# Kernel tuning notes

Hardware: AMD Instinct MI355X
Metric: run time of the kernel (lower is better)

The kernel has to match this reference:

```python
import jax, jax.numpy as jnp
import numpy as np

IN_FEATURES = 512
OUT_FEATURES = 512
GRID_SIZE = 5
SPLINE_ORDER = 3


def setup_inputs() -> dict:
    key = jax.random.key(0)
    k1, k2 = jax.random.split(key)
    x = jax.random.normal(k1, (8192, IN_FEATURES), dtype=jnp.float32)
    coefficients = jax.random.normal(
        k2, (IN_FEATURES, OUT_FEATURES, GRID_SIZE + SPLINE_ORDER), dtype=jnp.float32) * 0.1
    h = 2.0 / GRID_SIZE
    grid = jnp.linspace(-1.0 - SPLINE_ORDER * h, 1.0 + SPLINE_ORDER * h,
                        GRID_SIZE + 2 * SPLINE_ORDER + 1, dtype=jnp.float32)
    return {"x": x, "coefficients": coefficients, "grid": grid}


def _b_splines(xn, grid, order):
    # xn: (batch, in); grid: (G + 2*order + 1,)
    xe = xn[:, :, None]  # (b, i, 1)
    # k = 0: indicator of knot intervals -> (b, i, G + 2*order)
    B = ((xe >= grid[:-1]) & (xe < grid[1:])).astype(xn.dtype)
    for k in range(1, order + 1):
        left_den = grid[k:-1] - grid[:-k - 1]
        left_den = jnp.where(left_den == 0, jnp.ones_like(left_den), left_den)
        left = (xe - grid[:-k - 1]) / left_den * B[:, :, :-1]
        right_den = grid[k + 1:] - grid[1:-k]
        right_den = jnp.where(right_den == 0, jnp.ones_like(right_den), right_den)
        right = (grid[k + 1:] - xe) / right_den * B[:, :, 1:]
        B = left + right
    return B  # (b, i, G + order)


def reference(x, coefficients, grid):
    xn = jnp.tanh(x)
    bases = _b_splines(xn, grid, SPLINE_ORDER)  # (b, i, k)
    # replaces the double python loop: sum_i sum_k bases[b,i,k] * coeff[i,o,k]
    return jnp.einsum('bik,iok->bo', bases, coefficients)
```

## Files before the change

kernel.cpp:

```cpp
#include <hip/hip_runtime.h>
#include <hip/hip_bf16.h>
#include <stdint.h>


typedef short s16x8 __attribute__((ext_vector_type(8)));
typedef float f32x4 __attribute__((ext_vector_type(4)));

#define BATCH 8192
#define IN_F  512
#define OUT_F 512
#define NB    8
#define KKTOT (IN_F * NB)
#define BM 64
#define BN 128
#define BK 64
#define NITER (IN_F / NB)

__device__ __forceinline__ uint32_t f2bf(float f) {
    union { float f; uint32_t u; } v; v.f = f;
    return (v.u + 0x7FFFu + ((v.u >> 16) & 1u)) >> 16;
}

__device__ __forceinline__ uint32_t bf16bits(float a) {
    __hip_bfloat16 h = __float2bfloat16(a);
    union { __hip_bfloat16 h; unsigned short u; } c; c.h = h;
    return (uint32_t)c.u;
}

__device__ __forceinline__ s16x8 u4_to_s8(uint4 v) {
    union { uint4 u; s16x8 s; } c; c.u = v; return c.s;
}

__device__ __forceinline__ uint4 bspline_pack(float xraw) {
    float e  = __expf(2.0f * xraw);
    float xn = 1.0f - 2.0f / (e + 1.0f);
    float u  = __fmaf_rn(xn, 2.5f, 5.5f);
    float fj = floorf(u);
    fj = fminf(fmaxf(fj, 3.0f), 7.0f);
    float t  = u - fj;
    float omt = 1.0f - t;
    float t2 = t * t;
    float t3 = t2 * t;
    const float s = 0.16666666666666666f;
    float w0 = s * omt * omt * omt;
    float w3 = s * t3;
    float w1 = s * __fmaf_rn(3.0f, t3, __fmaf_rn(-6.0f, t2, 4.0f));
    float w2 = 1.0f - w0 - w1 - w3;
    uint64_t packed = (uint64_t)(bf16bits(w0) | (bf16bits(w1) << 16))
                    | ((uint64_t)(bf16bits(w2) | (bf16bits(w3) << 16)) << 32);
    int sh = ((int)fj - 3) * 16;
    uint64_t lo, hi;
    if (sh == 0)      { lo = packed;       hi = 0ull; }
    else if (sh < 64) { lo = packed << sh; hi = packed >> (64 - sh); }
    else              { lo = 0ull;         hi = packed; }
    return make_uint4((uint32_t)lo, (uint32_t)(lo >> 32),
                      (uint32_t)hi, (uint32_t)(hi >> 32));
}

__global__ __launch_bounds__(256)
void prep_bt(const float* __restrict__ C, unsigned short* __restrict__ BtT) {
    int t = blockIdx.x * 256 + threadIdx.x;
    int o = t & (OUT_F - 1);
    int i = t >> 9;
    const float4* src = (const float4*)(C + ((size_t)i * OUT_F + o) * NB);
    float4 c0 = src[0];
    float4 c1 = src[1];
    uint4 val;
    val.x = f2bf(c0.x) | (f2bf(c0.y) << 16);
    val.y = f2bf(c0.z) | (f2bf(c0.w) << 16);
    val.z = f2bf(c1.x) | (f2bf(c1.y) << 16);
    val.w = f2bf(c1.z) | (f2bf(c1.w) << 16);
    *(uint4*)(BtT + (size_t)o * KKTOT + (size_t)i * NB) = val;
}

__device__ __forceinline__ void gload_lds16(const void* g, void* l) {
    __builtin_amdgcn_global_load_lds(
        (const __attribute__((address_space(1))) uint32_t*)g,
        (__attribute__((address_space(3))) uint32_t*)l, 16, 0, 0);
}

__global__ __launch_bounds__(256, 2)
void kan_gemm(const float* __restrict__ X, const unsigned short* __restrict__ BtT,
              float* __restrict__ Out) {
    __shared__ unsigned short Bs[4][8192];

    const int tid    = threadIdx.x;
    const int lane   = tid & 63;
    const int wv     = tid >> 6;
    const int lane16 = lane & 15;
    const int quad   = lane >> 4;

    const int row0 = blockIdx.y * BM;
    const int col0 = blockIdx.x * BN;

    const float* xrow = X + (size_t)(row0 + wv * 16 + lane16) * IN_F;

    const int jg = (lane & 7) ^ ((lane >> 3) & 7);
    const char* gstage = (const char*)BtT
        + ((size_t)(col0 + wv * 8 + (lane >> 3))) * (KKTOT * 2)
        + (size_t)jg * 16;

    const int cbyte = lane16 * 128;
    const int sx0 = ((quad)     ^ (lane16 & 7)) << 4;
    const int sx1 = ((4 + quad) ^ (lane16 & 7)) << 4;

    f32x4 acc[8] = {};
    float xs0a, xs0b, xs1a, xs1b, xs2a, xs2b, xs3a, xs3b;

#define STAGE(BUF, T)                                                         \
    do {                                                                      \
        _Pragma("unroll")                                                     \
        for (int r = 0; r < 4; ++r)                                           \
            gload_lds16(gstage + (size_t)r * 32 * (KKTOT * 2) + (size_t)(T) * 128, \
                        (char*)&Bs[BUF][0] + r * 4096 + wv * 1024);           \
    } while (0)

    STAGE(0, 0);
    xs0a = xrow[quad];  xs0b = xrow[4 + quad];
    STAGE(1, 1);
    xs1a = xrow[8 + quad];  xs1b = xrow[12 + quad];
    asm volatile("s_waitcnt vmcnt(6)" ::: "memory");
    __builtin_amdgcn_s_barrier();

#define BODY(T, CUR, PRE, XCA, XCB, XPA, XPB)                                 \
    do {                                                                      \
        if ((T) + 2 < NITER) {                                                \
            STAGE(PRE, (T) + 2);                                              \
            XPA = xrow[((T) + 2) * 8 + quad];                                 \
            XPB = xrow[((T) + 2) * 8 + 4 + quad];                             \
        }                                                                     \
        const char* bsC = (const char*)&Bs[CUR][0];                           \
        {                                                                     \
            s16x8 af0 = u4_to_s8(bspline_pack(XCA));                          \
            _Pragma("unroll")                                                 \
            for (int cn = 0; cn < 8; ++cn) {                                  \
                s16x8 b = *(const s16x8*)(bsC + cn * 2048 + cbyte + sx0);     \
                acc[cn] = __builtin_amdgcn_mfma_f32_16x16x32_bf16(            \
                    af0, b, acc[cn], 0, 0, 0);                                \
            }                                                                 \
        }                                                                     \
        {                                                                     \
            s16x8 af1 = u4_to_s8(bspline_pack(XCB));                          \
            _Pragma("unroll")                                                 \
            for (int cn = 0; cn < 8; ++cn) {                                  \
                s16x8 b = *(const s16x8*)(bsC + cn * 2048 + cbyte + sx1);     \
                acc[cn] = __builtin_amdgcn_mfma_f32_16x16x32_bf16(            \
                    af1, b, acc[cn], 0, 0, 0);                                \
            }                                                                 \
        }                                                                     \
        if ((T) + 2 < NITER)                                                  \
            asm volatile("s_waitcnt vmcnt(6)" ::: "memory");                  \
        else if ((T) + 1 < NITER)                                             \
            asm volatile("s_waitcnt vmcnt(0)" ::: "memory");                  \
        if ((T) + 1 < NITER) __builtin_amdgcn_s_barrier();                    \
    } while (0)

    for (int t = 0; t < NITER; t += 4) {
        BODY(t + 0, 0, 2, xs0a, xs0b, xs2a, xs2b);
        BODY(t + 1, 1, 3, xs1a, xs1b, xs3a, xs3b);
        BODY(t + 2, 2, 0, xs2a, xs2b, xs0a, xs0b);
        BODY(t + 3, 3, 1, xs3a, xs3b, xs1a, xs1b);
    }
#undef BODY
#undef STAGE

    const int orow = row0 + wv * 16 + quad * 4;
    #pragma unroll
    for (int cn = 0; cn < 8; ++cn) {
        float* dst = Out + (size_t)orow * OUT_F + col0 + cn * 16 + lane16;
        #pragma unroll
        for (int r = 0; r < 4; ++r)
            dst[(size_t)r * OUT_F] = acc[cn][r];
    }
}

extern "C" void kernel_launch(void* const* d_in, const int* in_sizes, int n_in,
                              void* d_out, int out_size, void* d_ws, size_t ws_size,
                              hipStream_t stream) {
    const float* X  = (const float*)d_in[0];
    const float* C  = (const float*)d_in[1];
    float* Out = (float*)d_out;
    unsigned short* BtT = (unsigned short*)d_ws;

    prep_bt<<<dim3((IN_F * OUT_F) / 256), 256, 0, stream>>>(C, BtT);
    kan_gemm<<<dim3(OUT_F / BN, BATCH / BM), 256, 0, stream>>>(X, BtT, Out);
}
```

Before: 140.8 us.

## Use 2x2 wave tiling with paired-buffer prefetch in KAN spline GEMM

Reassigns the four waves from a 4x1 row split (16 rows by 128 columns each) to a 2x2 split (32 rows by 64 columns each). Each B fragment read from LDS now feeds two MFMAs, which halves LDS read traffic per MFMA. The cost is that every row's B-spline basis is now computed by two waves instead of one, doubling the tanh and basis arithmetic. The pipeline also changes: two stages are prefetched and consumed per barrier instead of one, so there are half as many barriers but each wait covers a larger batch of loads.

Measured after the change: 162.9 us. 15.7% more time.

```diff
diff --git a/kernel.cpp b/kernel.cpp
--- a/kernel.cpp
+++ b/kernel.cpp
@@ -87,25 +87,28 @@
     const int tid    = threadIdx.x;
     const int lane   = tid & 63;
     const int wv     = tid >> 6;
+    const int wr     = wv >> 1;
+    const int wc     = wv & 1;
     const int lane16 = lane & 15;
     const int quad   = lane >> 4;
 
     const int row0 = blockIdx.y * BM;
     const int col0 = blockIdx.x * BN;
 
-    const float* xrow = X + (size_t)(row0 + wv * 16 + lane16) * IN_F;
+    const float* xrA = X + (size_t)(row0 + wr * 32 + lane16) * IN_F;
+    const float* xrB = xrA + (size_t)16 * IN_F;
 
     const int jg = (lane & 7) ^ ((lane >> 3) & 7);
     const char* gstage = (const char*)BtT
         + ((size_t)(col0 + wv * 8 + (lane >> 3))) * (KKTOT * 2)
         + (size_t)jg * 16;
 
-    const int cbyte = lane16 * 128;
+    const int cwbyte = (wc * 64 + lane16) * 128;
     const int sx0 = ((quad)     ^ (lane16 & 7)) << 4;
     const int sx1 = ((4 + quad) ^ (lane16 & 7)) << 4;
 
-    f32x4 acc[8] = {};
-    float xs0a, xs0b, xs1a, xs1b, xs2a, xs2b, xs3a, xs3b;
+    f32x4 acc[2][4] = {};
+    float4 xv0, xv1, xv2, xv3;
 
 #define STAGE(BUF, T)                                                         \
     do {                                                                      \
@@ -115,62 +118,85 @@
                         (char*)&Bs[BUF][0] + r * 4096 + wv * 1024);           \
     } while (0)
 
-    STAGE(0, 0);
-    xs0a = xrow[quad];  xs0b = xrow[4 + quad];
-    STAGE(1, 1);
-    xs1a = xrow[8 + quad];  xs1b = xrow[12 + quad];
-    asm volatile("s_waitcnt vmcnt(6)" ::: "memory");
+#define XLOAD(XV, T)                                                          \
+    do {                                                                      \
+        XV.x = xrA[(T) * 8 + quad];                                           \
+        XV.y = xrA[(T) * 8 + 4 + quad];                                       \
+        XV.z = xrB[(T) * 8 + quad];                                           \
+        XV.w = xrB[(T) * 8 + 4 + quad];                                       \
+    } while (0)
+
+#define TILE(CUR, XV)                                                         \
+    do {                                                                      \
+        const char* bs_ = (const char*)&Bs[CUR][0] + cwbyte;                  \
+        s16x8 b[4];                                                           \
+        s16x8 af;                                                             \
+        _Pragma("unroll")                                                     \
+        for (int cn = 0; cn < 4; ++cn)                                        \
+            b[cn] = *(const s16x8*)(bs_ + cn * 2048 + sx0);                   \
+        af = u4_to_s8(bspline_pack(XV.x));                                    \
+        _Pragma("unroll")                                                     \
+        for (int cn = 0; cn < 4; ++cn)                                        \
+            acc[0][cn] = __builtin_amdgcn_mfma_f32_16x16x32_bf16(             \
+                af, b[cn], acc[0][cn], 0, 0, 0);                              \
+        af = u4_to_s8(bspline_pack(XV.z));                                    \
+        _Pragma("unroll")                                                     \
+        for (int cn = 0; cn < 4; ++cn)                                        \
+            acc[1][cn] = __builtin_amdgcn_mfma_f32_16x16x32_bf16(             \
+                af, b[cn], acc[1][cn], 0, 0, 0);                              \
+        _Pragma("unroll")                                                     \
+        for (int cn = 0; cn < 4; ++cn)                                        \
+            b[cn] = *(const s16x8*)(bs_ + cn * 2048 + sx1);                   \
+        af = u4_to_s8(bspline_pack(XV.y));                                    \
+        _Pragma("unroll")                                                     \
+        for (int cn = 0; cn < 4; ++cn)                                        \
+            acc[0][cn] = __builtin_amdgcn_mfma_f32_16x16x32_bf16(             \
+                af, b[cn], acc[0][cn], 0, 0, 0);                              \
+        af = u4_to_s8(bspline_pack(XV.w));                                    \
+        _Pragma("unroll")                                                     \
+        for (int cn = 0; cn < 4; ++cn)                                        \
+            acc[1][cn] = __builtin_amdgcn_mfma_f32_16x16x32_bf16(             \
+                af, b[cn], acc[1][cn], 0, 0, 0);                              \
+    } while (0)
+
+    STAGE(0, 0); XLOAD(xv0, 0);
+    STAGE(1, 1); XLOAD(xv1, 1);
+    asm volatile("s_waitcnt vmcnt(4)" ::: "memory");
     __builtin_amdgcn_s_barrier();
 
-#define BODY(T, CUR, PRE, XCA, XCB, XPA, XPB)                                 \
-    do {                                                                      \
-        if ((T) + 2 < NITER) {                                                \
-            STAGE(PRE, (T) + 2);                                              \
-            XPA = xrow[((T) + 2) * 8 + quad];                                 \
-            XPB = xrow[((T) + 2) * 8 + 4 + quad];                             \
-        }                                                                     \
-        const char* bsC = (const char*)&Bs[CUR][0];                           \
-        {                                                                     \
-            s16x8 af0 = u4_to_s8(bspline_pack(XCA));                          \
-            _Pragma("unroll")                                                 \
-            for (int cn = 0; cn < 8; ++cn) {                                  \
-                s16x8 b = *(const s16x8*)(bsC + cn * 2048 + cbyte + sx0);     \
-                acc[cn] = __builtin_amdgcn_mfma_f32_16x16x32_bf16(            \
-                    af0, b, acc[cn], 0, 0, 0);                                \
-            }                                                                 \
-        }                                                                     \
-        {                                                                     \
-            s16x8 af1 = u4_to_s8(bspline_pack(XCB));                          \
-            _Pragma("unroll")                                                 \
-            for (int cn = 0; cn < 8; ++cn) {                                  \
-                s16x8 b = *(const s16x8*)(bsC + cn * 2048 + cbyte + sx1);     \
-                acc[cn] = __builtin_amdgcn_mfma_f32_16x16x32_bf16(            \
-                    af1, b, acc[cn], 0, 0, 0);                                \
-            }                                                                 \
-        }                                                                     \
-        if ((T) + 2 < NITER)                                                  \
-            asm volatile("s_waitcnt vmcnt(6)" ::: "memory");                  \
-        else if ((T) + 1 < NITER)                                             \
-            asm volatile("s_waitcnt vmcnt(0)" ::: "memory");                  \
-        if ((T) + 1 < NITER) __builtin_amdgcn_s_barrier();                    \
-    } while (0)
-
     for (int t = 0; t < NITER; t += 4) {
-        BODY(t + 0, 0, 2, xs0a, xs0b, xs2a, xs2b);
-        BODY(t + 1, 1, 3, xs1a, xs1b, xs3a, xs3b);
-        BODY(t + 2, 2, 0, xs2a, xs2b, xs0a, xs0b);
-        BODY(t + 3, 3, 1, xs3a, xs3b, xs1a, xs1b);
+        STAGE(2, t + 2); XLOAD(xv2, t + 2);
+        STAGE(3, t + 3); XLOAD(xv3, t + 3);
+        TILE(0, xv0);
+        TILE(1, xv1);
+        asm volatile("s_waitcnt vmcnt(4)" ::: "memory");
+        __builtin_amdgcn_s_barrier();
+
+        if (t + 4 < NITER) {
+            STAGE(0, t + 4); XLOAD(xv0, t + 4);
+            STAGE(1, t + 5); XLOAD(xv1, t + 5);
+        }
+        TILE(2, xv2);
+        TILE(3, xv3);
+        if (t + 4 < NITER) {
+            asm volatile("s_waitcnt vmcnt(4)" ::: "memory");
+            __builtin_amdgcn_s_barrier();
+        }
     }
-#undef BODY
+#undef TILE
+#undef XLOAD
 #undef STAGE
 
-    const int orow = row0 + wv * 16 + quad * 4;
     #pragma unroll
-    for (int cn = 0; cn < 8; ++cn) {
-        float* dst = Out + (size_t)orow * OUT_F + col0 + cn * 16 + lane16;
+    for (int rm = 0; rm < 2; ++rm) {
+        const int orow = row0 + wr * 32 + rm * 16 + quad * 4;
         #pragma unroll
-        for (int r = 0; r < 4; ++r)
-            dst[(size_t)r * OUT_F] = acc[cn][r];
+        for (int cn = 0; cn < 4; ++cn) {
+            float* dst = Out + (size_t)orow * OUT_F + col0 + wc * 64 + cn * 16 + lane16;
+            #pragma unroll
+            for (int r = 0; r < 4; ++r)
+                dst[(size_t)r * OUT_F] = acc[rm][cn][r];
+        }
     }
 }
 
```

## Materialize B-spline basis matrix once and run plain bf16 GEMM

Applied to the files above, without the earlier changes.

Adds a pack_a kernel that evaluates the tanh and cubic B-spline basis for every input once and writes a bf16 A matrix (8192x4096) to workspace. A new GEMM kernel then streams both A and B tiles into LDS with a 2x2 wave layout and double buffering. This removes the basis recomputation that the fused kernel did in every block along the output-column dimension. In exchange it adds 64 MB of writes plus reads of the A matrix, and the new GEMM waits on vmcnt(0) each step. The fused kernel is kept as a fallback when the workspace is too small.

Measured after the change: 140.5 us. About the same (-0.2%).

```diff
diff --git a/kernel.cpp b/kernel.cpp
--- a/kernel.cpp
+++ b/kernel.cpp
@@ -73,6 +73,19 @@
     *(uint4*)(BtT + (size_t)o * KKTOT + (size_t)i * NB) = val;
 }
 
+__global__ __launch_bounds__(256)
+void pack_a(const float* __restrict__ X, unsigned short* __restrict__ Abf) {
+    int t = blockIdx.x * 256 + threadIdx.x;
+    int b  = t >> 8;
+    int ip = t & 255;
+    float2 xv = *(const float2*)(X + (size_t)b * IN_F + ip * 2);
+    uint4 p0 = bspline_pack(xv.x);
+    uint4 p1 = bspline_pack(xv.y);
+    unsigned short* dst = Abf + (size_t)b * KKTOT + ip * 16;
+    *(uint4*)(dst)     = p0;
+    *(uint4*)(dst + 8) = p1;
+}
+
 __device__ __forceinline__ void gload_lds16(const void* g, void* l) {
     __builtin_amdgcn_global_load_lds(
         (const __attribute__((address_space(1))) uint32_t*)g,
@@ -80,8 +93,118 @@
 }
 
 __global__ __launch_bounds__(256, 2)
-void kan_gemm(const float* __restrict__ X, const unsigned short* __restrict__ BtT,
-              float* __restrict__ Out) {
+void kan_gemm_mat(const unsigned short* __restrict__ Abf,
+                  const unsigned short* __restrict__ BtT,
+                  float* __restrict__ Out) {
+    __shared__ unsigned short As[2][4096];
+    __shared__ unsigned short Bs[2][8192];
+
+    const int tid    = threadIdx.x;
+    const int lane   = tid & 63;
+    const int wv     = tid >> 6;
+    const int wr     = wv >> 1;
+    const int wc     = wv & 1;
+    const int lane16 = lane & 15;
+    const int quad   = lane >> 4;
+
+    const int row0 = blockIdx.y * BM;
+    const int col0 = blockIdx.x * BN;
+
+    const int jg = (lane & 7) ^ ((lane >> 3) & 7);
+    const char* gstageB = (const char*)BtT
+        + ((size_t)(col0 + wv * 8 + (lane >> 3))) * (KKTOT * 2)
+        + (size_t)jg * 16;
+    const char* gstageA = (const char*)Abf
+        + ((size_t)(row0 + wv * 8 + (lane >> 3))) * (KKTOT * 2)
+        + (size_t)jg * 16;
+
+    const int cwbyte = (wc * 64 + lane16) * 128;
+    const int arbyte = (wr * 32 + lane16) * 128;
+    const int sx0 = ((quad)     ^ (lane16 & 7)) << 4;
+    const int sx1 = ((4 + quad) ^ (lane16 & 7)) << 4;
+
+    f32x4 acc[2][4] = {};
+
+#define STAGE(BUF, T)                                                         \
+    do {                                                                      \
+        _Pragma("unroll")                                                     \
+        for (int r = 0; r < 4; ++r)                                           \
+            gload_lds16(gstageB + (size_t)r * 32 * (KKTOT * 2) + (size_t)(T) * 128, \
+                        (char*)&Bs[BUF][0] + r * 4096 + wv * 1024);           \
+        gload_lds16(gstageA + (size_t)(T) * 128,                              \
+                    (char*)&As[BUF][0] + wv * 1024);                          \
+        gload_lds16(gstageA + (size_t)32 * (KKTOT * 2) + (size_t)(T) * 128,   \
+                    (char*)&As[BUF][0] + 4096 + wv * 1024);                   \
+    } while (0)
+
+#define TILE(CUR)                                                             \
+    do {                                                                      \
+        const char* bs_ = (const char*)&Bs[CUR][0] + cwbyte;                  \
+        const char* as_ = (const char*)&As[CUR][0] + arbyte;                  \
+        s16x8 b0, b1, b2, b3, af0, af1;                                       \
+        af0 = *(const s16x8*)(as_ + sx0);                                     \
+        af1 = *(const s16x8*)(as_ + 2048 + sx0);                              \
+        b0 = *(const s16x8*)(bs_ + 0 * 2048 + sx0);                           \
+        b1 = *(const s16x8*)(bs_ + 1 * 2048 + sx0);                           \
+        b2 = *(const s16x8*)(bs_ + 2 * 2048 + sx0);                           \
+        b3 = *(const s16x8*)(bs_ + 3 * 2048 + sx0);                           \
+        acc[0][0] = __builtin_amdgcn_mfma_f32_16x16x32_bf16(af0, b0, acc[0][0], 0, 0, 0); \
+        acc[0][1] = __builtin_amdgcn_mfma_f32_16x16x32_bf16(af0, b1, acc[0][1], 0, 0, 0); \
+        acc[0][2] = __builtin_amdgcn_mfma_f32_16x16x32_bf16(af0, b2, acc[0][2], 0, 0, 0); \
+        acc[0][3] = __builtin_amdgcn_mfma_f32_16x16x32_bf16(af0, b3, acc[0][3], 0, 0, 0); \
+        acc[1][0] = __builtin_amdgcn_mfma_f32_16x16x32_bf16(af1, b0, acc[1][0], 0, 0, 0); \
+        acc[1][1] = __builtin_amdgcn_mfma_f32_16x16x32_bf16(af1, b1, acc[1][1], 0, 0, 0); \
+        acc[1][2] = __builtin_amdgcn_mfma_f32_16x16x32_bf16(af1, b2, acc[1][2], 0, 0, 0); \
+        acc[1][3] = __builtin_amdgcn_mfma_f32_16x16x32_bf16(af1, b3, acc[1][3], 0, 0, 0); \
+        af0 = *(const s16x8*)(as_ + sx1);                                     \
+        af1 = *(const s16x8*)(as_ + 2048 + sx1);                              \
+        b0 = *(const s16x8*)(bs_ + 0 * 2048 + sx1);                           \
+        b1 = *(const s16x8*)(bs_ + 1 * 2048 + sx1);                           \
+        b2 = *(const s16x8*)(bs_ + 2 * 2048 + sx1);                           \
+        b3 = *(const s16x8*)(bs_ + 3 * 2048 + sx1);                           \
+        acc[0][0] = __builtin_amdgcn_mfma_f32_16x16x32_bf16(af0, b0, acc[0][0], 0, 0, 0); \
+        acc[0][1] = __builtin_amdgcn_mfma_f32_16x16x32_bf16(af0, b1, acc[0][1], 0, 0, 0); \
+        acc[0][2] = __builtin_amdgcn_mfma_f32_16x16x32_bf16(af0, b2, acc[0][2], 0, 0, 0); \
+        acc[0][3] = __builtin_amdgcn_mfma_f32_16x16x32_bf16(af0, b3, acc[0][3], 0, 0, 0); \
+        acc[1][0] = __builtin_amdgcn_mfma_f32_16x16x32_bf16(af1, b0, acc[1][0], 0, 0, 0); \
+        acc[1][1] = __builtin_amdgcn_mfma_f32_16x16x32_bf16(af1, b1, acc[1][1], 0, 0, 0); \
+        acc[1][2] = __builtin_amdgcn_mfma_f32_16x16x32_bf16(af1, b2, acc[1][2], 0, 0, 0); \
+        acc[1][3] = __builtin_amdgcn_mfma_f32_16x16x32_bf16(af1, b3, acc[1][3], 0, 0, 0); \
+    } while (0)
+
+    STAGE(0, 0);
+    asm volatile("s_waitcnt vmcnt(0)" ::: "memory");
+    __builtin_amdgcn_s_barrier();
+
+    for (int t = 0; t < NITER; t += 2) {
+        if (t + 1 < NITER) STAGE(1, t + 1);
+        TILE(0);
+        asm volatile("s_waitcnt vmcnt(0)" ::: "memory");
+        __builtin_amdgcn_s_barrier();
+        if (t + 2 < NITER) STAGE(0, t + 2);
+        TILE(1);
+        asm volatile("s_waitcnt vmcnt(0)" ::: "memory");
+        __builtin_amdgcn_s_barrier();
+    }
+#undef TILE
+#undef STAGE
+
+    #pragma unroll
+    for (int rm = 0; rm < 2; ++rm) {
+        const int orow = row0 + wr * 32 + rm * 16 + quad * 4;
+        #pragma unroll
+        for (int cn = 0; cn < 4; ++cn) {
+            float* dst = Out + (size_t)orow * OUT_F + col0 + wc * 64 + cn * 16 + lane16;
+            #pragma unroll
+            for (int r = 0; r < 4; ++r)
+                dst[(size_t)r * OUT_F] = acc[rm][cn][r];
+        }
+    }
+}
+
+__global__ __launch_bounds__(256, 2)
+void kan_gemm_fused(const float* __restrict__ X, const unsigned short* __restrict__ BtT,
+                    float* __restrict__ Out) {
     __shared__ unsigned short Bs[4][8192];
 
     const int tid    = threadIdx.x;
@@ -107,7 +230,7 @@
     f32x4 acc[8] = {};
     float xs0a, xs0b, xs1a, xs1b, xs2a, xs2b, xs3a, xs3b;
 
-#define STAGE(BUF, T)                                                         \
+#define FSTAGE(BUF, T)                                                        \
     do {                                                                      \
         _Pragma("unroll")                                                     \
         for (int r = 0; r < 4; ++r)                                           \
@@ -115,17 +238,17 @@
                         (char*)&Bs[BUF][0] + r * 4096 + wv * 1024);           \
     } while (0)
 
-    STAGE(0, 0);
+    FSTAGE(0, 0);
     xs0a = xrow[quad];  xs0b = xrow[4 + quad];
-    STAGE(1, 1);
+    FSTAGE(1, 1);
     xs1a = xrow[8 + quad];  xs1b = xrow[12 + quad];
     asm volatile("s_waitcnt vmcnt(6)" ::: "memory");
     __builtin_amdgcn_s_barrier();
 
-#define BODY(T, CUR, PRE, XCA, XCB, XPA, XPB)                                 \
+#define FBODY(T, CUR, PRE, XCA, XCB, XPA, XPB)                                \
     do {                                                                      \
         if ((T) + 2 < NITER) {                                                \
-            STAGE(PRE, (T) + 2);                                              \
+            FSTAGE(PRE, (T) + 2);                                             \
             XPA = xrow[((T) + 2) * 8 + quad];                                 \
             XPB = xrow[((T) + 2) * 8 + 4 + quad];                             \
         }                                                                     \
@@ -156,13 +279,13 @@
     } while (0)
 
     for (int t = 0; t < NITER; t += 4) {
-        BODY(t + 0, 0, 2, xs0a, xs0b, xs2a, xs2b);
-        BODY(t + 1, 1, 3, xs1a, xs1b, xs3a, xs3b);
-        BODY(t + 2, 2, 0, xs2a, xs2b, xs0a, xs0b);
-        BODY(t + 3, 3, 1, xs3a, xs3b, xs1a, xs1b);
-    }
-#undef BODY
-#undef STAGE
+        FBODY(t + 0, 0, 2, xs0a, xs0b, xs2a, xs2b);
+        FBODY(t + 1, 1, 3, xs1a, xs1b, xs3a, xs3b);
+        FBODY(t + 2, 2, 0, xs2a, xs2b, xs0a, xs0b);
+        FBODY(t + 3, 3, 1, xs3a, xs3b, xs1a, xs1b);
+    }
+#undef FBODY
+#undef FSTAGE
 
     const int orow = row0 + wv * 16 + quad * 4;
     #pragma unroll
@@ -180,8 +303,18 @@
     const float* X  = (const float*)d_in[0];
     const float* C  = (const float*)d_in[1];
     float* Out = (float*)d_out;
+
+    const size_t needB = (size_t)OUT_F * KKTOT * 2;
+    const size_t needA = (size_t)BATCH * KKTOT * 2;
+
     unsigned short* BtT = (unsigned short*)d_ws;
-
     prep_bt<<<dim3((IN_F * OUT_F) / 256), 256, 0, stream>>>(C, BtT);
-    kan_gemm<<<dim3(OUT_F / BN, BATCH / BM), 256, 0, stream>>>(X, BtT, Out);
-}
+
+    if (ws_size >= needB + needA) {
+        unsigned short* Abf = (unsigned short*)((char*)d_ws + needB);
+        pack_a<<<dim3((BATCH * IN_F / 2) / 256), 256, 0, stream>>>(X, Abf);
+        kan_gemm_mat<<<dim3(OUT_F / BN, BATCH / BM), 256, 0, stream>>>(Abf, BtT, Out);
+    } else {
+        kan_gemm_fused<<<dim3(OUT_F / BN, BATCH / BM), 256, 0, stream>>>(X, BtT, Out);
+    }
+}
```
